# Performance work log

Measured on AMD Instinct MI355X. Metric: run time of the kernel, lower is better.

Reference implementation:

```python
import jax, jax.numpy as jnp
import numpy as np

DIM = 1024
L = 10
C = 1.0
SQRT_C = float(np.sqrt(C))


def _exp_map(x, v, c):
    # Poincare exp map (general form, as in the torch source)
    xn2 = jnp.sum(x * x, axis=-1, keepdims=True)
    lam = 2.0 / (1.0 - c * xn2)
    vn = jnp.sqrt(jnp.sum(v * v, axis=-1, keepdims=True))
    vn = jnp.maximum(vn, 1e-8)
    second = jnp.tanh(SQRT_C * lam * vn / 2.0) / (SQRT_C * vn) * v
    num = (1.0 - c * xn2) * second
    den = (1.0 - 2.0 * c * jnp.sum(x * second, axis=-1, keepdims=True)
           + c * c * xn2 * jnp.sum(second * second, axis=-1, keepdims=True))
    return x + num / den


def _log_map(x, y, c):
    # Poincare log map (general form, as in the torch source)
    xn2 = jnp.sum(x * x, axis=-1, keepdims=True)
    lam = 2.0 / (1.0 - c * xn2)
    yn2 = jnp.sum(y * y, axis=-1, keepdims=True)
    xy = jnp.sum(x * y, axis=-1, keepdims=True)
    tv = (-x * yn2 + y * (1.0 + c * xn2) - 2.0 * c * xy * x) / (1.0 - c * xn2)
    tn = jnp.sqrt(jnp.sum(tv * tv, axis=-1, keepdims=True))
    num = 2.0 * SQRT_C * jnp.arctanh(SQRT_C * tn)
    den = SQRT_C * lam * tn
    return num / den * tv


def _butterfly(u, params):
    # Stage l: blocks of size 2^l along the feature dim; within each block,
    # adjacent pairs are rotated by that block's (a, b) Givens-like rotation.
    # Param layout matches __init__: for layer l there are dim>>l blocks,
    # 2 params (a, b) each, laid out contiguously layer after layer.
    B = u.shape[0]
    offset = 0
    for l in range(L):
        bs = 1 << l
        nb = DIM // bs
        seg = params[offset:offset + 2 * nb]
        offset += 2 * nb
        if bs < 2:
            continue  # block of size 1 has no pair to rotate
        ab = seg.reshape(nb, 2)
        a = ab[:, 0][None, :, None]  # [1, nb, 1]
        b = ab[:, 1][None, :, None]
        u4 = u.reshape(B, nb, bs // 2, 2)
        u0 = u4[..., 0]
        u1 = u4[..., 1]
        u = jnp.stack([a * u0 + b * u1, -b * u0 + a * u1], axis=-1).reshape(B, DIM)
    return u


def setup_inputs() -> dict:
    key = jax.random.key(0)
    k1, k2 = jax.random.split(key)
    # points inside the Poincare ball: per-row norm ~ 0.01*sqrt(1024) ~ 0.32
    x = jax.random.normal(k1, (32768, DIM), dtype=jnp.float32) * 0.01
    P = 2 * sum(DIM >> l for l in range(L))  # 4092
    base = jnp.tile(jnp.array([0.9, 0.0], dtype=jnp.float32), P // 2)
    params = base + 0.1 * jax.random.normal(k2, (P,), dtype=jnp.float32)
    return {"x": x, "params": params}


def reference(x, params):
    u = _log_map(jnp.zeros_like(x), x, C)
    u = _butterfly(u, params)
    return _exp_map(jnp.zeros_like(u), u, C)
```

## Files before the change

kernel.cpp:

```cpp
#include <hip/hip_runtime.h>
#include <math.h>

#define DIM 1024
#define NPAIRS 512
#define NLEVELS 9

__global__ void butterfly_weights_kernel(const float* __restrict__ params,
                                         float2* __restrict__ w) {
    int p = blockIdx.x * blockDim.x + threadIdx.x;
    if (p >= NPAIRS) return;
    float wr = 1.0f, wi = 0.0f;
    int off = 2 * DIM;
#pragma unroll
    for (int l = 1; l <= NLEVELS; ++l) {
        int j = p >> (l - 1);
        float a = params[off + 2 * j];
        float b = params[off + 2 * j + 1];
        float nr = wr * a + wi * b;
        float ni = wi * a - wr * b;
        wr = nr;
        wi = ni;
        off += 2 * (DIM >> l);
    }
    w[p] = make_float2(wr, wi);
}

__global__ __launch_bounds__(256) void hyper_butterfly_wave_kernel(
        const float* __restrict__ x,
        const float4* __restrict__ w4,
        float* __restrict__ out,
        int rows) {
    const int lane = threadIdx.x & 63;
    const int wave = threadIdx.x >> 6;
    const int row = blockIdx.x * 4 + wave;
    if (row >= rows) return;

    const float4* xrow = (const float4*)(x + (size_t)row * DIM);

    float4 xv[4], wv[4];
#pragma unroll
    for (int i = 0; i < 4; ++i) {
        xv[i] = xrow[lane + 64 * i];
        wv[i] = w4[lane + 64 * i];
    }

    float p1 = 0.0f, p2 = 0.0f;
#pragma unroll
    for (int i = 0; i < 4; ++i) {
        float a0 = xv[i].x * xv[i].x + xv[i].y * xv[i].y;
        float a1 = xv[i].z * xv[i].z + xv[i].w * xv[i].w;
        float m0 = wv[i].x * wv[i].x + wv[i].y * wv[i].y;
        float m1 = wv[i].z * wv[i].z + wv[i].w * wv[i].w;
        p1 += a0 + a1;
        p2 += m0 * a0 + m1 * a1;
    }

#pragma unroll
    for (int o = 32; o > 0; o >>= 1) {
        p1 += __shfl_xor(p1, o);
        p2 += __shfl_xor(p2, o);
    }

    float r = sqrtf(p1);
    float s1 = (r > 1e-12f) ? (0.5f * logf((1.0f + r) / (1.0f - r)) / r)
                            : 1.0f;
    float vn = fmaxf(s1 * sqrtf(p2), 1e-8f);
    float s2 = tanhf(vn) / vn;
    float s = s1 * s2;

    float4* orow = (float4*)(out + (size_t)row * DIM);
#pragma unroll
    for (int i = 0; i < 4; ++i) {
        float4 o4;
        o4.x = s * (wv[i].x * xv[i].x - wv[i].y * xv[i].y);
        o4.y = s * (wv[i].x * xv[i].y + wv[i].y * xv[i].x);
        o4.z = s * (wv[i].z * xv[i].z - wv[i].w * xv[i].w);
        o4.w = s * (wv[i].z * xv[i].w + wv[i].w * xv[i].z);
        orow[lane + 64 * i] = o4;
    }
}

extern "C" void kernel_launch(void* const* d_in, const int* in_sizes, int n_in,
                              void* d_out, int out_size, void* d_ws, size_t ws_size,
                              hipStream_t stream) {
    const float* x = (const float*)d_in[0];
    const float* params = (const float*)d_in[1];
    float* out = (float*)d_out;
    float2* w = (float2*)d_ws;

    int rows = in_sizes[0] / DIM;

    butterfly_weights_kernel<<<1, NPAIRS, 0, stream>>>(params, w);

    int blocks = (rows + 3) / 4;
    hyper_butterfly_wave_kernel<<<blocks, 256, 0, stream>>>(
        x, (const float4*)w, out, rows);
}
```

Measured before the change: 228.9 us.

## Fuse butterfly weight computation into main kernel and use nontemporal stores

Removes the separate single-block weights kernel and has every wave recompute the per-pair complex weights directly from params, which eliminates one launch and the dependency between the two kernels. Output stores become nontemporal to avoid polluting cache with streaming writes. The trade-off is redundant per-wave arithmetic and many small param loads, which should mostly hit cache.

```diff
diff --git a/kernel.cpp b/kernel.cpp
--- a/kernel.cpp
+++ b/kernel.cpp
@@ -3,31 +3,12 @@
 
 #define DIM 1024
 #define NPAIRS 512
-#define NLEVELS 9
 
-__global__ void butterfly_weights_kernel(const float* __restrict__ params,
-                                         float2* __restrict__ w) {
-    int p = blockIdx.x * blockDim.x + threadIdx.x;
-    if (p >= NPAIRS) return;
-    float wr = 1.0f, wi = 0.0f;
-    int off = 2 * DIM;
-#pragma unroll
-    for (int l = 1; l <= NLEVELS; ++l) {
-        int j = p >> (l - 1);
-        float a = params[off + 2 * j];
-        float b = params[off + 2 * j + 1];
-        float nr = wr * a + wi * b;
-        float ni = wi * a - wr * b;
-        wr = nr;
-        wi = ni;
-        off += 2 * (DIM >> l);
-    }
-    w[p] = make_float2(wr, wi);
-}
+typedef float f32x4 __attribute__((ext_vector_type(4)));
 
-__global__ __launch_bounds__(256) void hyper_butterfly_wave_kernel(
+__global__ __launch_bounds__(256) void hyper_butterfly_fused_kernel(
         const float* __restrict__ x,
-        const float4* __restrict__ w4,
+        const float* __restrict__ params,
         float* __restrict__ out,
         int rows) {
     const int lane = threadIdx.x & 63;
@@ -36,12 +17,31 @@
     if (row >= rows) return;
 
     const float4* xrow = (const float4*)(x + (size_t)row * DIM);
+    float4 xv[4];
+#pragma unroll
+    for (int i = 0; i < 4; ++i) xv[i] = xrow[lane + 64 * i];
 
-    float4 xv[4], wv[4];
+    const float2* pf2 = (const float2*)params;
+    float4 wv[4];
 #pragma unroll
     for (int i = 0; i < 4; ++i) {
-        xv[i] = xrow[lane + 64 * i];
-        wv[i] = w4[lane + 64 * i];
+        const int q = lane + 64 * i;
+        float cr = 1.0f, ci = 0.0f;
+        const int F[8] = {1536, 1792, 1920, 1984, 2016, 2032, 2040, 2044};
+#pragma unroll
+        for (int l = 0; l < 8; ++l) {
+            float2 ab = pf2[F[l] + (q >> l)];
+            float nr = cr * ab.x + ci * ab.y;
+            float ni = ci * ab.x - cr * ab.y;
+            cr = nr;
+            ci = ni;
+        }
+        float2 ab0 = pf2[1024 + 2 * q];
+        float2 ab1 = pf2[1024 + 2 * q + 1];
+        wv[i].x = cr * ab0.x + ci * ab0.y;
+        wv[i].y = ci * ab0.x - cr * ab0.y;
+        wv[i].z = cr * ab1.x + ci * ab1.y;
+        wv[i].w = ci * ab1.x - cr * ab1.y;
     }
 
     float p1 = 0.0f, p2 = 0.0f;
@@ -65,18 +65,17 @@
     float s1 = (r > 1e-12f) ? (0.5f * logf((1.0f + r) / (1.0f - r)) / r)
                             : 1.0f;
     float vn = fmaxf(s1 * sqrtf(p2), 1e-8f);
-    float s2 = tanhf(vn) / vn;
-    float s = s1 * s2;
+    float s = s1 * (tanhf(vn) / vn);
 
-    float4* orow = (float4*)(out + (size_t)row * DIM);
+    f32x4* orow = (f32x4*)(out + (size_t)row * DIM);
 #pragma unroll
     for (int i = 0; i < 4; ++i) {
-        float4 o4;
+        f32x4 o4;
         o4.x = s * (wv[i].x * xv[i].x - wv[i].y * xv[i].y);
         o4.y = s * (wv[i].x * xv[i].y + wv[i].y * xv[i].x);
         o4.z = s * (wv[i].z * xv[i].z - wv[i].w * xv[i].w);
         o4.w = s * (wv[i].z * xv[i].w + wv[i].w * xv[i].z);
-        orow[lane + 64 * i] = o4;
+        __builtin_nontemporal_store(o4, &orow[lane + 64 * i]);
     }
 }
 
@@ -86,13 +85,10 @@
     const float* x = (const float*)d_in[0];
     const float* params = (const float*)d_in[1];
     float* out = (float*)d_out;
-    float2* w = (float2*)d_ws;
 
     int rows = in_sizes[0] / DIM;
 
-    butterfly_weights_kernel<<<1, NPAIRS, 0, stream>>>(params, w);
-
     int blocks = (rows + 3) / 4;
-    hyper_butterfly_wave_kernel<<<blocks, 256, 0, stream>>>(
-        x, (const float4*)w, out, rows);
+    hyper_butterfly_fused_kernel<<<blocks, 256, 0, stream>>>(
+        x, params, out, rows);
 }
```

Result: slower. 233.8 us (+2.2%).
